# Optimization experiments

Measured on AMD Instinct MI355X. Metric: run time of the kernel, lower is better.

The kernel has to match this reference:

```python
import jax, jax.numpy as jnp
import numpy as np

B, S, E, H, V = 64, 256, 300, 300, 30000
R, NREL, RELD, POL = 512, 46, 50, 3


def setup_inputs() -> dict:
    rng = np.random.RandomState(0)
    text_indices = rng.randint(1, V, size=(B, S)).astype(np.int64)  # all nonzero -> text_len == S
    aspect_indices = rng.randint(1, V, size=(B, 4)).astype(np.int64)  # aspect_len == 4
    left_indices = np.zeros((B, 64), dtype=np.int64)
    for b in range(B):
        li = rng.randint(1, 61)
        left_indices[b, :li] = rng.randint(1, V, size=li)
    # distinct, row-major-sorted (head, behead) pairs so nonzero(adj) order matches relation order
    flat = np.stack([np.sort(rng.choice(S * S, size=R, replace=False)) for _ in range(B)])
    head = (flat // S).astype(np.int64)
    behead = (flat % S).astype(np.int64)
    relation = rng.randint(1, NREL, size=(B, R)).astype(np.int64)  # all nonzero
    adj = np.zeros((B, S, S), dtype=np.float32)
    adj[np.arange(B)[:, None], head, behead] = 1.0

    def p(*shape):
        return jnp.asarray((rng.randn(*shape) * 0.02).astype(np.float32))

    rel_embed = np.asarray(rng.randn(NREL, RELD) * 0.02, dtype=np.float32)
    rel_embed[0] = 0.0  # padding_idx=0
    return dict(
        text_indices=jnp.asarray(text_indices),
        aspect_indices=jnp.asarray(aspect_indices),
        left_indices=jnp.asarray(left_indices),
        adj=jnp.asarray(adj),
        head_vector=jnp.asarray(head),
        behead_vector=jnp.asarray(behead),
        relation_vector=jnp.asarray(relation),
        embed_table=p(V, E),
        rel_embed=jnp.asarray(rel_embed),
        Wf_ih=p(4 * H, E), Wf_hh=p(4 * H, H), bf=p(4 * H),
        Wb_ih=p(4 * H, E), Wb_hh=p(4 * H, H), bb=p(4 * H),
        bil_W=p(4 * H, RELD), bil_b=p(1),
        gc1_W=p(2 * H, 2 * H), gc1_b=p(2 * H),
        gc2_W=p(2 * H, 2 * H), gc2_b=p(2 * H),
        fc_W=p(2 * H, POL), fc_b=p(POL),
    )


def _lstm_dir(x_tbe, W_ih, W_hh, b):
    # x_tbe: [S, B, E]; PyTorch gate order i, f, g, o
    def step(carry, xt):
        h, c = carry
        g = xt @ W_ih.T + h @ W_hh.T + b
        i, f, gg, o = jnp.split(g, 4, axis=-1)
        c = jax.nn.sigmoid(f) * c + jax.nn.sigmoid(i) * jnp.tanh(gg)
        h = jax.nn.sigmoid(o) * jnp.tanh(c)
        return (h, c), h
    nb = x_tbe.shape[1]
    init = (jnp.zeros((nb, H), x_tbe.dtype), jnp.zeros((nb, H), x_tbe.dtype))
    _, hs = jax.lax.scan(step, init, x_tbe)
    return hs


def _bilstm(x, Wf_ih, Wf_hh, bf, Wb_ih, Wb_hh, bb):
    xt = jnp.swapaxes(x, 0, 1)  # [S, B, E]; all lengths == S by construction
    hf = _lstm_dir(xt, Wf_ih, Wf_hh, bf)
    hb = _lstm_dir(xt[::-1], Wb_ih, Wb_hh, bb)[::-1]
    return jnp.swapaxes(jnp.concatenate([hf, hb], axis=-1), 0, 1)  # [B, S, 2H]


def _pos_weight(x, l0, l1, text_len, aspect_len):
    j = jnp.arange(S, dtype=jnp.float32)[None, :]
    tl = text_len.astype(jnp.float32)[:, None]
    ctx = tl - aspect_len.astype(jnp.float32)[:, None]
    l0f = l0.astype(jnp.float32)[:, None]
    l1f = l1.astype(jnp.float32)[:, None]
    w = jnp.where(j < l0f, 1.0 - (l0f - j) / ctx,
        jnp.where(j <= l1f, 0.0,
        jnp.where(j < tl, 1.0 - (j - l1f) / ctx, 0.0)))
    return w[:, :, None] * x


def _gcn(text, adj, W, b):
    hidden = text @ W
    denom = jnp.sum(adj, axis=2, keepdims=True) + 1.0
    return jnp.matmul(adj, hidden) / denom + b


def reference(text_indices, aspect_indices, left_indices, adj, head_vector,
              behead_vector, relation_vector, embed_table, rel_embed,
              Wf_ih, Wf_hh, bf, Wb_ih, Wb_hh, bb, bil_W, bil_b,
              gc1_W, gc1_b, gc2_W, gc2_b, fc_W, fc_b):
    text_len = jnp.sum(text_indices != 0, axis=-1)
    aspect_len = jnp.sum(aspect_indices != 0, axis=-1)
    left_len = jnp.sum(left_indices != 0, axis=-1)
    l0 = left_len
    l1 = left_len + aspect_len - 1

    text = embed_table[text_indices]  # dropout is identity in eval mode
    text_out = _bilstm(text, Wf_ih, Wf_hh, bf, Wb_ih, Wb_hh, bb)  # [B, S, 2H]

    # --- word_relation_word: gather head/tail nodes, bilinear score, scatter into adj ---
    bidx = jnp.arange(B)[:, None]
    ind = (relation_vector != 0).astype(text_out.dtype)[:, :, None]
    node1 = jnp.where(ind != 0, text_out[bidx, head_vector], ind)   # [B, R, 2H]
    node2 = jnp.where(ind != 0, text_out[bidx, behead_vector], ind)
    ww = jnp.concatenate([node1, node2], axis=-1)                   # [B, R, 4H]
    ef = rel_embed[relation_vector]                                 # [B, R, 50]
    score = jax.nn.sigmoid(jnp.einsum('bri,ij,brj->br', ww, bil_W, ef) + bil_b[0])
    # nonzero(adj) positions == (head, behead) pairs in row-major order by construction
    adj = adj.at[bidx, head_vector, behead_vector].set(score)

    x = jax.nn.relu(_gcn(_pos_weight(text_out, l0, l1, text_len, aspect_len), adj, gc1_W, gc1_b))
    x = jax.nn.relu(_gcn(_pos_weight(x, l0, l1, text_len, aspect_len), adj, gc2_W, gc2_b))

    j = jnp.arange(S)[None, :]
    m = ((j >= l0[:, None]) & (j <= l1[:, None])).astype(x.dtype)[:, :, None]
    x = m * x
    alpha_mat = jnp.matmul(x, jnp.swapaxes(text_out, 1, 2))  # [B, S, S]
    alpha = jax.nn.softmax(jnp.sum(alpha_mat, axis=1, keepdims=True), axis=2)
    x = jnp.matmul(alpha, text_out).squeeze(1)               # [B, 2H]
    return x @ fc_W + fc_b
```

## Files before the change

kernel.cpp:

```cpp
#include <hip/hip_runtime.h>
#include <hip/hip_bf16.h>

typedef __hip_bfloat16 bf16;
using f32x4 = __attribute__((ext_vector_type(4))) float;
using s16x8 = __attribute__((ext_vector_type(8))) short;

#define DEV __device__ __forceinline__
DEV float bf2f(bf16 x) { return __bfloat162float(x); }
DEV bf16  f2bf(float x) { return __float2bfloat16(x); }
DEV ushort f2bu(float x) { bf16 h = __float2bfloat16(x); return *(ushort*)&h; }
DEV float fsig(float x)  { return 1.f / (1.f + __expf(-x)); }
DEV float ftanh(float x) {
    float xc = fminf(fmaxf(x, -15.f), 15.f);
    float e = __expf(2.f * xc);
    return (e - 1.f) / (e + 1.f);
}

#define BB 64
#define SS 256
#define EE 300
#define HH 300
#define H2 600
#define G4 1200
#define RR 512
#define VV 30000

#define NWG 25
#define CPW 12
#define HPITCH 304

#define SLOTSZ   19660800ul
#define GATES_SZ 39321600ul
#define OFF_TEXT  39321600ul
#define OFF_ADJ   78643200ul
#define OFF_P     87031808ul
#define OFF_DENOM 87252608ul
#define OFF_POSW  87318144ul
#define OFF_L0L1  87383680ul
#define OFF_W1T   87384704ul
#define OFF_W2T   88104704ul
#define OFF_HG    88824704ul
#define OFF_FLAGS 88980352ul
#define SEQ_END   89045888ul
#define CONC_END  128367488ul

struct __attribute__((packed, aligned(4))) u16x8v { ushort v[8]; };

__global__ void k_init_denom(float* denom) {
    int i = blockIdx.x * 256 + threadIdx.x;
    if (i < BB * SS) denom[i] = 1.f;
}

__global__ void k_lengths(const int* __restrict__ text_idx,
                          const int* __restrict__ aspect_idx,
                          const int* __restrict__ left_idx,
                          int* __restrict__ l0l1, float* __restrict__ posw) {
    int b = blockIdx.x, tid = threadIdx.x;
    __shared__ int cnt[3];
    if (tid < 3) cnt[tid] = 0;
    __syncthreads();
    if (text_idx[b * SS + tid] != 0) atomicAdd(&cnt[0], 1);
    if (tid < 4 && aspect_idx[b * 4 + tid] != 0) atomicAdd(&cnt[1], 1);
    if (tid < 64 && left_idx[b * 64 + tid] != 0) atomicAdd(&cnt[2], 1);
    __syncthreads();
    int tl = cnt[0], al = cnt[1], ll = cnt[2];
    int l0 = ll, l1 = ll + al - 1;
    if (tid == 0) { l0l1[b * 2] = l0; l0l1[b * 2 + 1] = l1; }
    float ctx = fmaxf((float)(tl - al), 1.f);
    float j = (float)tid, l0f = (float)l0, l1f = (float)l1, tlf = (float)tl;
    float w;
    if (j < l0f)       w = 1.f - (l0f - j) / ctx;
    else if (j <= l1f) w = 0.f;
    else if (j < tlf)  w = 1.f - (j - l1f) / ctx;
    else               w = 0.f;
    posw[b * SS + tid] = w;
}

__global__ void k_P(const float* __restrict__ bilW, const float* __restrict__ relE,
                    float* __restrict__ P) {
    int id = blockIdx.x * 256 + threadIdx.x;
    if (id >= G4 * 46) return;
    int i = id / 46, r = id % 46;
    float s = 0.f;
    for (int j = 0; j < 50; ++j) s += bilW[i * 50 + j] * relE[r * 50 + j];
    P[id] = s;
}

__global__ void k_transpose600(const float* __restrict__ W, bf16* __restrict__ WT) {
    int id = blockIdx.x * 256 + threadIdx.x;
    if (id >= H2 * H2) return;
    int n = id / H2, k = id % H2;
    WT[id] = f2bf(W[k * H2 + n]);
}

__global__ void k_pw1(const float* __restrict__ text_out, const float* __restrict__ posw,
                      bf16* __restrict__ pw1) {
    int id = blockIdx.x * 256 + threadIdx.x;
    if (id >= 16384 * H2) return;
    int m = id / H2;
    pw1[id] = f2bf(posw[m] * text_out[id]);
}

template<int EPI, bool GATHER_A, bool BATCHED, bool CVT>
__global__ __launch_bounds__(256) void gemm_bt(
    const void* __restrict__ Abv, const void* __restrict__ Bbv,
    int M, int N, int K, int lda, int ldb, long sA, long sB,
    const int* __restrict__ gidx,
    const float* __restrict__ bias0,
    const float* __restrict__ denom, const float* __restrict__ posw,
    bf16* __restrict__ Cbf, int ldc)
{
    __shared__ __align__(16) ushort As[128 * 40];
    __shared__ __align__(16) ushort Bs[128 * 40];
    const int tid  = threadIdx.x;
    const int lane = tid & 63, wave = tid >> 6;
    const int wm = (wave >> 1) * 64, wn = (wave & 1) * 64;
    const int mt = blockIdx.x * 128, nt = blockIdx.y * 128;
    const int z  = BATCHED ? blockIdx.z : 0;

    const int srow = tid >> 1;
    const int kseg = (tid & 1) * 16;
    long arow = mt + srow;
    if (GATHER_A) {
        int g = gidx[mt + srow];
        if (g < 0 || g >= VV) g = 0;
        arow = g;
    }
    const int nrow = nt + srow;
    const bool bval = nrow < N;
    const int nrc = bval ? nrow : 0;

    const ushort* Ap16 = nullptr; const ushort* Bp16 = nullptr;
    const float*  Ap32 = nullptr; const float*  Bp32 = nullptr;
    if (CVT) {
        Ap32 = (const float*)Abv + (BATCHED ? (long)z * sA : 0l) + arow * (long)lda;
        Bp32 = (const float*)Bbv + (BATCHED ? (long)z * sB : 0l) + (long)nrc * ldb;
    } else {
        Ap16 = (const ushort*)Abv + (BATCHED ? (long)z * sA : 0l) + arow * (long)lda;
        Bp16 = (const ushort*)Bbv + (BATCHED ? (long)z * sB : 0l) + (long)nrc * ldb;
    }

    f32x4 acc[4][4];
#pragma unroll
    for (int i = 0; i < 4; ++i)
#pragma unroll
        for (int j = 0; j < 4; ++j) acc[i][j] = (f32x4){0.f, 0.f, 0.f, 0.f};

    for (int k0 = 0; k0 < K; k0 += 32) {
        __syncthreads();
#pragma unroll
        for (int hv = 0; hv < 2; ++hv) {
            const int kk = k0 + kseg + hv * 8;
            union { ushort u[8]; uint4 q; } ta, tb;
            if (CVT) {
                if (kk + 8 <= K) {
                    float4 f0 = *(const float4*)(Ap32 + kk);
                    float4 f1 = *(const float4*)(Ap32 + kk + 4);
                    ta.u[0] = f2bu(f0.x); ta.u[1] = f2bu(f0.y); ta.u[2] = f2bu(f0.z); ta.u[3] = f2bu(f0.w);
                    ta.u[4] = f2bu(f1.x); ta.u[5] = f2bu(f1.y); ta.u[6] = f2bu(f1.z); ta.u[7] = f2bu(f1.w);
                } else {
#pragma unroll
                    for (int i2 = 0; i2 < 8; ++i2) ta.u[i2] = (kk + i2 < K) ? f2bu(Ap32[kk + i2]) : (ushort)0;
                }
                if (bval && kk + 8 <= K) {
                    float4 f0 = *(const float4*)(Bp32 + kk);
                    float4 f1 = *(const float4*)(Bp32 + kk + 4);
                    tb.u[0] = f2bu(f0.x); tb.u[1] = f2bu(f0.y); tb.u[2] = f2bu(f0.z); tb.u[3] = f2bu(f0.w);
                    tb.u[4] = f2bu(f1.x); tb.u[5] = f2bu(f1.y); tb.u[6] = f2bu(f1.z); tb.u[7] = f2bu(f1.w);
                } else {
#pragma unroll
                    for (int i2 = 0; i2 < 8; ++i2) tb.u[i2] = (bval && kk + i2 < K) ? f2bu(Bp32[kk + i2]) : (ushort)0;
                }
            } else {
                if (kk + 8 <= K) {
                    u16x8v v = *(const u16x8v*)(Ap16 + kk);
#pragma unroll
                    for (int i2 = 0; i2 < 8; ++i2) ta.u[i2] = v.v[i2];
                } else {
#pragma unroll
                    for (int i2 = 0; i2 < 8; ++i2) ta.u[i2] = (kk + i2 < K) ? Ap16[kk + i2] : (ushort)0;
                }
                if (bval && kk + 8 <= K) {
                    u16x8v v = *(const u16x8v*)(Bp16 + kk);
#pragma unroll
                    for (int i2 = 0; i2 < 8; ++i2) tb.u[i2] = v.v[i2];
                } else {
#pragma unroll
                    for (int i2 = 0; i2 < 8; ++i2) tb.u[i2] = (bval && kk + i2 < K) ? Bp16[kk + i2] : (ushort)0;
                }
            }
            *(uint4*)&As[srow * 40 + kseg + hv * 8] = ta.q;
            *(uint4*)&Bs[srow * 40 + kseg + hv * 8] = tb.q;
        }
        __syncthreads();
        s16x8 af[4], bfr[4];
#pragma unroll
        for (int i = 0; i < 4; ++i)
            af[i] = *(const s16x8*)&As[(wm + i * 16 + (lane & 15)) * 40 + (lane >> 4) * 8];
#pragma unroll
        for (int j = 0; j < 4; ++j)
            bfr[j] = *(const s16x8*)&Bs[(wn + j * 16 + (lane & 15)) * 40 + (lane >> 4) * 8];
#pragma unroll
        for (int i = 0; i < 4; ++i)
#pragma unroll
            for (int j = 0; j < 4; ++j)
                acc[i][j] = __builtin_amdgcn_mfma_f32_16x16x32_bf16(af[i], bfr[j], acc[i][j], 0, 0, 0);
    }

#pragma unroll
    for (int i = 0; i < 4; ++i) {
        const int rm = mt + wm + i * 16 + ((lane >> 4) * 4);
#pragma unroll
        for (int j = 0; j < 4; ++j) {
            const int gn = nt + wn + j * 16 + (lane & 15);
            if (gn >= N) continue;
#pragma unroll
            for (int r = 0; r < 4; ++r) {
                const int gm = rm + r;
                const float v = acc[i][j][r];
                if (EPI == 0) {
                    const int bb2 = gm >> 8, tt2 = gm & 255;
                    const int g3 = gn / 300, gr = gn % 300;
                    const int wgq = gr / 12, jq = gr % 12;
                    Cbf[(((long)tt2 * NWG + wgq) * BB + bb2) * 48 + g3 * 12 + jq]
                        = f2bf(v + bias0[gn]);
                } else if (EPI == 1) {
                    const int bb2 = gm >> 8, jj = gm & 255;
                    Cbf[((long)bb2 * H2 + gn) * SS + jj] = f2bf(v);
                } else {
                    const int grow = z * SS + gm;
                    float v2 = v / denom[grow] + bias0[gn];
                    v2 = fmaxf(v2, 0.f);
                    if (EPI == 2) v2 *= posw[grow];
                    Cbf[(long)grow * ldc + gn] = f2bf(v2);
                }
            }
        }
    }
}

__global__ __launch_bounds__(256, 1) void k_lstm_mfma(
    const bf16* __restrict__ gatesF, const bf16* __restrict__ gatesB,
    const float* __restrict__ WhhF, const float* __restrict__ WhhB,
    bf16* __restrict__ hgbase,
    int* __restrict__ flagbase,
    float* __restrict__ text_out, int dir_base)
{
    const int dir = dir_base + blockIdx.x / NWG;
    const int wg  = blockIdx.x % NWG;
    const ushort* gu  = (const ushort*)(dir ? gatesB : gatesF);
    const float*  Whh = dir ? WhhB : WhhF;
    ushort* hg   = (ushort*)hgbase + (long)dir * (2 * 64 * HPITCH);
    int*   flags = flagbase + dir * (256 * 32);

    const int tid = threadIdx.x, lane = tid & 63, wave = tid >> 6;
    __shared__ float cbuf[64 * CPW];

    const int nl15 = lane & 15;
    const int kq = lane >> 4;
    const int gI = nl15 & 3;
    s16x8 Bfrag[3][10];
#pragma unroll
    for (int tt = 0; tt < 3; ++tt) {
        const int j = (tt * 16 + nl15) >> 2;
        const float* wrow = Whh + ((long)(gI * HH + wg * CPW + j)) * HH;
        const int kb = kq * 8;
        for (int ss = 0; ss < 10; ++ss) {
            union { ushort u[8]; s16x8 v; } tb;
#pragma unroll
            for (int e = 0; e < 8; ++e) {
                const int k = ss * 32 + kb + e;
                tb.u[e] = (k < HH) ? f2bu(wrow[k]) : (ushort)0;
            }
            Bfrag[tt][ss] = tb.v;
        }
    }
    for (int i = tid; i < 64 * CPW; i += 256) cbuf[i] = 0.f;
    __syncthreads();

    const int am = wave * 16 + nl15;

    ushort gcur[3][4], gnxt[3][4];
    {
        const int tcur = dir ? (SS - 1) : 0;
#pragma unroll
        for (int tt = 0; tt < 3; ++tt) {
            const int col48 = gI * 12 + ((tt * 16 + nl15) >> 2);
#pragma unroll
            for (int r = 0; r < 4; ++r) {
                const int mb = wave * 16 + (kq << 2) + r;
                gcur[tt][r] = gu[(((long)tcur * NWG + wg) * BB + mb) * 48 + col48];
            }
        }
    }

    for (int s = 0; s < SS; ++s) {
        const int t = dir ? (SS - 1 - s) : s;
        const int rb = s & 1;
        unsigned long long hq[20];
        {
            const unsigned long long* src =
                (const unsigned long long*)(hg + rb * (64 * HPITCH)) + (long)am * 76;
#pragma unroll
            for (int ss = 0; ss < 10; ++ss) {
                hq[2 * ss]     = __hip_atomic_load(&src[ss * 8 + kq * 2],
                                                   __ATOMIC_RELAXED, __HIP_MEMORY_SCOPE_AGENT);
                hq[2 * ss + 1] = __hip_atomic_load(&src[ss * 8 + kq * 2 + 1],
                                                   __ATOMIC_RELAXED, __HIP_MEMORY_SCOPE_AGENT);
            }
        }
        f32x4 acc[3];
#pragma unroll
        for (int tt = 0; tt < 3; ++tt) acc[tt] = (f32x4){0.f, 0.f, 0.f, 0.f};
#pragma unroll
        for (int ss = 0; ss < 10; ++ss) {
            union { unsigned long long q[2]; s16x8 v; } ua;
            ua.q[0] = hq[2 * ss]; ua.q[1] = hq[2 * ss + 1];
#pragma unroll
            for (int tt = 0; tt < 3; ++tt)
                acc[tt] = __builtin_amdgcn_mfma_f32_16x16x32_bf16(ua.v, Bfrag[tt][ss], acc[tt], 0, 0, 0);
        }
        ushort* hw = hg + (rb ^ 1) * (64 * HPITCH);
#pragma unroll
        for (int tt = 0; tt < 3; ++tt) {
            const int j = (tt * 16 + nl15) >> 2;
            const int hc = wg * CPW + j;
#pragma unroll
            for (int r = 0; r < 4; ++r) {
                const int mb = wave * 16 + (kq << 2) + r;
                const bf16 gb = *(const bf16*)&gcur[tt][r];
                const float val = acc[tt][r] + bf2f(gb);
                const float a = (gI == 2) ? ftanh(val) : fsig(val);
                const float v1 = __shfl_xor(a, 1);
                const float v2 = __shfl_xor(a, 2);
                const float v3 = __shfl_xor(a, 3);
                if (gI == 0) {
                    const int ci = mb * CPW + j;
                    const float c = v1 * cbuf[ci] + a * v2;
                    cbuf[ci] = c;
                    const float h = v3 * ftanh(c);
                    bf16 hb = f2bf(h);
                    __hip_atomic_store(&hw[mb * HPITCH + hc], *(ushort*)&hb,
                                       __ATOMIC_RELAXED, __HIP_MEMORY_SCOPE_AGENT);
                    text_out[((long)(mb * SS + t)) * H2 + dir * HH + hc] = h;
                }
            }
        }
        if (s == SS - 1) break;
        __syncthreads();
        if (tid == 0)
            __hip_atomic_store(&flags[s * 32 + wg], 1, __ATOMIC_RELAXED, __HIP_MEMORY_SCOPE_AGENT);
        {
            const int tn = dir ? (SS - 2 - s) : (s + 1);
#pragma unroll
            for (int tt = 0; tt < 3; ++tt) {
                const int col48 = gI * 12 + ((tt * 16 + nl15) >> 2);
#pragma unroll
                for (int r = 0; r < 4; ++r) {
                    const int mb = wave * 16 + (kq << 2) + r;
                    gnxt[tt][r] = gu[(((long)tn * NWG + wg) * BB + mb) * 48 + col48];
                }
            }
        }
        if (tid < NWG) {
            while (__hip_atomic_load(&flags[s * 32 + tid], __ATOMIC_RELAXED,
                                     __HIP_MEMORY_SCOPE_AGENT) == 0) { }
        }
        __syncthreads();
#pragma unroll
        for (int tt = 0; tt < 3; ++tt)
#pragma unroll
            for (int r = 0; r < 4; ++r) gcur[tt][r] = gnxt[tt][r];
    }
}

__global__ void k_scores(const float* __restrict__ text_out, const float* __restrict__ P,
                         const int* __restrict__ head, const int* __restrict__ behead,
                         const int* __restrict__ rel, const float* __restrict__ bil_b,
                         bf16* __restrict__ adj, float* __restrict__ denom)
{
    const int gw = (blockIdx.x * blockDim.x + threadIdx.x) >> 6;
    const int lane = threadIdx.x & 63;
    if (gw >= BB * RR) return;
    const int b = gw >> 9, r = gw & 511;
    int rl = rel[b * RR + r];     if (rl < 0 || rl > 45) rl = 0;
    int hd = head[b * RR + r]   & 255;
    int bh = behead[b * RR + r] & 255;
    const float* n1 = text_out + ((long)(b * SS + hd)) * H2;
    const float* n2 = text_out + ((long)(b * SS + bh)) * H2;
    float part = 0.f;
    for (int i = lane; i < H2; i += 64) {
        part += n1[i] * P[(long)i * 46 + rl];
        part += n2[i] * P[(long)(H2 + i) * 46 + rl];
    }
    for (int off = 32; off; off >>= 1) part += __shfl_down(part, off);
    if (lane == 0) {
        const float sc = 1.f / (1.f + expf(-(part + bil_b[0])));
        adj[((long)(b * SS + hd)) * SS + bh] = f2bf(sc);
        atomicAdd(&denom[b * SS + hd], sc);
    }
}

__global__ __launch_bounds__(256) void k_attn(
    const float* __restrict__ text_out, const bf16* __restrict__ x2,
    const int* __restrict__ l0l1, const float* __restrict__ fcW,
    const float* __restrict__ fcb, float* __restrict__ out)
{
    const int b = blockIdx.x, tid = threadIdx.x;
    const int wave = tid >> 6, lane = tid & 63;
    __shared__ float xs[H2];
    __shared__ float sc[SS];
    __shared__ float red[16];
    const int l0 = l0l1[b * 2], l1 = l0l1[b * 2 + 1];
    for (int n = tid; n < H2; n += 256) {
        float s = 0.f;
        for (int i = l0; i <= l1 && i < SS; ++i) s += bf2f(x2[((long)(b * SS + i)) * H2 + n]);
        xs[n] = s;
    }
    __syncthreads();
    for (int j = wave; j < SS; j += 4) {
        const float* row = text_out + ((long)(b * SS + j)) * H2;
        float p = 0.f;
        for (int n = lane; n < H2; n += 64) p += xs[n] * row[n];
        for (int off = 32; off; off >>= 1) p += __shfl_down(p, off);
        if (lane == 0) sc[j] = p;
    }
    __syncthreads();
    const float v = sc[tid];
    float mx = v;
    for (int off = 32; off; off >>= 1) mx = fmaxf(mx, __shfl_down(mx, off));
    if (lane == 0) red[wave] = mx;
    __syncthreads();
    if (tid == 0) red[8] = fmaxf(fmaxf(red[0], red[1]), fmaxf(red[2], red[3]));
    __syncthreads();
    const float e = expf(v - red[8]);
    sc[tid] = e;
    float sm = e;
    for (int off = 32; off; off >>= 1) sm += __shfl_down(sm, off);
    if (lane == 0) red[wave] = sm;
    __syncthreads();
    if (tid == 0) red[9] = red[0] + red[1] + red[2] + red[3];
    __syncthreads();
    const float inv = 1.f / red[9];
    for (int n = tid; n < H2; n += 256) {
        float a = 0.f;
        for (int j = 0; j < SS; ++j) a += sc[j] * text_out[((long)(b * SS + j)) * H2 + n];
        xs[n] = a * inv;
    }
    __syncthreads();
    if (wave < 3) {
        float p = 0.f;
        for (int n = lane; n < H2; n += 64) p += xs[n] * fcW[n * 3 + wave];
        for (int off = 32; off; off >>= 1) p += __shfl_down(p, off);
        if (lane == 0) out[b * 3 + wave] = p + fcb[wave];
    }
}

extern "C" void kernel_launch(void* const* d_in, const int* in_sizes, int n_in,
                              void* d_out, int out_size, void* d_ws, size_t ws_size,
                              hipStream_t stream) {
    const int*   text_idx   = (const int*)d_in[0];
    const int*   aspect_idx = (const int*)d_in[1];
    const int*   left_idx   = (const int*)d_in[2];
    const int*   head       = (const int*)d_in[4];
    const int*   behead     = (const int*)d_in[5];
    const int*   rel        = (const int*)d_in[6];
    const float* embed      = (const float*)d_in[7];
    const float* relE       = (const float*)d_in[8];
    const float* Wf_ih      = (const float*)d_in[9];
    const float* Wf_hh      = (const float*)d_in[10];
    const float* bf_b       = (const float*)d_in[11];
    const float* Wb_ih      = (const float*)d_in[12];
    const float* Wb_hh      = (const float*)d_in[13];
    const float* bb_b       = (const float*)d_in[14];
    const float* bilW       = (const float*)d_in[15];
    const float* bilb       = (const float*)d_in[16];
    const float* gc1W       = (const float*)d_in[17];
    const float* gc1b       = (const float*)d_in[18];
    const float* gc2W       = (const float*)d_in[19];
    const float* gc2b       = (const float*)d_in[20];
    const float* fcW        = (const float*)d_in[21];
    const float* fcb        = (const float*)d_in[22];

    const bool  conc  = ws_size >= CONC_END;
    const size_t base2 = conc ? GATES_SZ : 0ul;

    char* ws = (char*)d_ws;
    bf16*  gatesF   = (bf16*)(ws);
    bf16*  gatesB   = conc ? (bf16*)(ws + GATES_SZ) : gatesF;
    bf16*  slot0bf  = (bf16*)(ws);
    bf16*  slot1bf  = (bf16*)(ws + SLOTSZ);
    float* text_out = (float*)(ws + OFF_TEXT  + base2);
    bf16*  adjw     = (bf16*)(ws + OFF_ADJ    + base2);
    float* P        = (float*)(ws + OFF_P     + base2);
    float* denom    = (float*)(ws + OFF_DENOM + base2);
    float* posw     = (float*)(ws + OFF_POSW  + base2);
    int*   l0l1     = (int*)(ws + OFF_L0L1    + base2);
    bf16*  W1T      = (bf16*)(ws + OFF_W1T    + base2);
    bf16*  W2T      = (bf16*)(ws + OFF_W2T    + base2);
    bf16*  hgbase   = (bf16*)(ws + OFF_HG     + base2);
    int*   flagbase = (int*)(ws + OFF_FLAGS   + base2);

    dim3 blk(256);

    hipMemsetAsync(adjw, 0, (size_t)BB * SS * SS * 2, stream);
    hipMemsetAsync(hgbase, 0, 155648 + 65536, stream);
    k_init_denom<<<64, blk, 0, stream>>>(denom);
    k_lengths<<<64, blk, 0, stream>>>(text_idx, aspect_idx, left_idx, l0l1, posw);
    k_P<<<(G4 * 46 + 255) / 256, blk, 0, stream>>>(bilW, relE, P);
    k_transpose600<<<(H2 * H2 + 255) / 256, blk, 0, stream>>>(gc1W, W1T);
    k_transpose600<<<(H2 * H2 + 255) / 256, blk, 0, stream>>>(gc2W, W2T);

    if (conc) {
        gemm_bt<0, true, false, true><<<dim3(128, 10), blk, 0, stream>>>(
            embed, Wf_ih, 16384, G4, EE, EE, EE, 0, 0,
            text_idx, bf_b, nullptr, nullptr, gatesF, G4);
        gemm_bt<0, true, false, true><<<dim3(128, 10), blk, 0, stream>>>(
            embed, Wb_ih, 16384, G4, EE, EE, EE, 0, 0,
            text_idx, bb_b, nullptr, nullptr, gatesB, G4);
        k_lstm_mfma<<<2 * NWG, blk, 0, stream>>>(
            gatesF, gatesB, Wf_hh, Wb_hh, hgbase, flagbase, text_out, 0);
    } else {
        gemm_bt<0, true, false, true><<<dim3(128, 10), blk, 0, stream>>>(
            embed, Wf_ih, 16384, G4, EE, EE, EE, 0, 0,
            text_idx, bf_b, nullptr, nullptr, gatesF, G4);
        k_lstm_mfma<<<NWG, blk, 0, stream>>>(
            gatesF, gatesB, Wf_hh, Wb_hh, hgbase, flagbase, text_out, 0);
        gemm_bt<0, true, false, true><<<dim3(128, 10), blk, 0, stream>>>(
            embed, Wb_ih, 16384, G4, EE, EE, EE, 0, 0,
            text_idx, bb_b, nullptr, nullptr, gatesB, G4);
        k_lstm_mfma<<<NWG, blk, 0, stream>>>(
            gatesF, gatesB, Wf_hh, Wb_hh, hgbase, flagbase, text_out, 1);
    }

    k_scores<<<(BB * RR * 64 + 255) / 256, blk, 0, stream>>>(
        text_out, P, head, behead, rel, bilb, adjw, denom);
    k_pw1<<<(16384 * H2 + 255) / 256, blk, 0, stream>>>(text_out, posw, slot0bf);

    gemm_bt<1, false, false, false><<<dim3(128, 5), blk, 0, stream>>>(
        slot0bf, W1T, 16384, H2, H2, H2, H2, 0, 0,
        nullptr, nullptr, nullptr, nullptr, slot1bf, 0);
    gemm_bt<2, false, true, false><<<dim3(2, 5, 64), blk, 0, stream>>>(
        adjw, slot1bf, SS, H2, SS, SS, SS, (long)SS * SS, (long)H2 * SS,
        nullptr, gc1b, denom, posw, slot0bf, H2);
    gemm_bt<1, false, false, false><<<dim3(128, 5), blk, 0, stream>>>(
        slot0bf, W2T, 16384, H2, H2, H2, H2, 0, 0,
        nullptr, nullptr, nullptr, nullptr, slot1bf, 0);
    gemm_bt<3, false, true, false><<<dim3(2, 5, 64), blk, 0, stream>>>(
        adjw, slot1bf, SS, H2, SS, SS, SS, (long)SS * SS, (long)H2 * SS,
        nullptr, gc2b, denom, posw, slot0bf, H2);

    k_attn<<<64, blk, 0, stream>>>(text_out, slot0bf, l0l1, fcW, fcb, (float*)d_out);
}
```

Before: 2.087 ms.

## Fuse setup kernels, merge gate GEMMs, fold pos-weight into GEMM, register LSTM cell

Folds the denom init into k_lengths and merges the two weight transposes into one launch. The forward and backward input-gate GEMMs become a single launch over 2*G4 columns, with per-column routing of bias and destination. The separate k_pw1 pass goes away: posw scaling and the bf16 conversion now happen in the first GCN GEMM's A-load through a new ASCALE path. In the LSTM, cell state moves from shared memory into registers, and the flag signal is raised before the text_out global stores so peers can proceed sooner. These changes cut launches and one full activation round trip, at the cost of more template complexity and more register pressure in the LSTM.

```diff
diff --git a/kernel.cpp b/kernel.cpp
--- a/kernel.cpp
+++ b/kernel.cpp
@@ -46,15 +46,11 @@
 
 struct __attribute__((packed, aligned(4))) u16x8v { ushort v[8]; };
 
-__global__ void k_init_denom(float* denom) {
-    int i = blockIdx.x * 256 + threadIdx.x;
-    if (i < BB * SS) denom[i] = 1.f;
-}
-
 __global__ void k_lengths(const int* __restrict__ text_idx,
                           const int* __restrict__ aspect_idx,
                           const int* __restrict__ left_idx,
-                          int* __restrict__ l0l1, float* __restrict__ posw) {
+                          int* __restrict__ l0l1, float* __restrict__ posw,
+                          float* __restrict__ denom) {
     int b = blockIdx.x, tid = threadIdx.x;
     __shared__ int cnt[3];
     if (tid < 3) cnt[tid] = 0;
@@ -74,6 +70,7 @@
     else if (j < tlf)  w = 1.f - (j - l1f) / ctx;
     else               w = 0.f;
     posw[b * SS + tid] = w;
+    denom[b * SS + tid] = 1.f;
 }
 
 __global__ void k_P(const float* __restrict__ bilW, const float* __restrict__ relE,
@@ -86,29 +83,26 @@
     P[id] = s;
 }
 
-__global__ void k_transpose600(const float* __restrict__ W, bf16* __restrict__ WT) {
+__global__ void k_transpose2(const float* __restrict__ Wa, const float* __restrict__ Wb,
+                             bf16* __restrict__ Ta, bf16* __restrict__ Tb) {
     int id = blockIdx.x * 256 + threadIdx.x;
-    if (id >= H2 * H2) return;
-    int n = id / H2, k = id % H2;
-    WT[id] = f2bf(W[k * H2 + n]);
-}
-
-__global__ void k_pw1(const float* __restrict__ text_out, const float* __restrict__ posw,
-                      bf16* __restrict__ pw1) {
-    int id = blockIdx.x * 256 + threadIdx.x;
-    if (id >= 16384 * H2) return;
-    int m = id / H2;
-    pw1[id] = f2bf(posw[m] * text_out[id]);
-}
-
-template<int EPI, bool GATHER_A, bool BATCHED, bool CVT>
+    if (id >= 2 * H2 * H2) return;
+    const float* W = (id < H2 * H2) ? Wa : Wb;
+    bf16* T = (id < H2 * H2) ? Ta : Tb;
+    int l = (id < H2 * H2) ? id : id - H2 * H2;
+    int n = l / H2, k = l % H2;
+    T[l] = f2bf(W[k * H2 + n]);
+}
+
+template<int EPI, bool GATHER_A, bool BATCHED, bool CVTA, bool CVTB, bool ASCALE>
 __global__ __launch_bounds__(256) void gemm_bt(
-    const void* __restrict__ Abv, const void* __restrict__ Bbv,
+    const void* __restrict__ Abv, const void* __restrict__ Bbv, const void* __restrict__ B2v,
     int M, int N, int K, int lda, int ldb, long sA, long sB,
     const int* __restrict__ gidx,
-    const float* __restrict__ bias0,
+    const float* __restrict__ bias0, const float* __restrict__ bias1,
+    const float* __restrict__ ascale,
     const float* __restrict__ denom, const float* __restrict__ posw,
-    bf16* __restrict__ Cbf, int ldc)
+    bf16* __restrict__ Cbf, bf16* __restrict__ Cbf2, int ldc)
 {
     __shared__ __align__(16) ushort As[128 * 40];
     __shared__ __align__(16) ushort Bs[128 * 40];
@@ -132,13 +126,22 @@
 
     const ushort* Ap16 = nullptr; const ushort* Bp16 = nullptr;
     const float*  Ap32 = nullptr; const float*  Bp32 = nullptr;
-    if (CVT) {
+    if (CVTA) {
         Ap32 = (const float*)Abv + (BATCHED ? (long)z * sA : 0l) + arow * (long)lda;
-        Bp32 = (const float*)Bbv + (BATCHED ? (long)z * sB : 0l) + (long)nrc * ldb;
     } else {
         Ap16 = (const ushort*)Abv + (BATCHED ? (long)z * sA : 0l) + arow * (long)lda;
+    }
+    if (CVTB) {
+        if (EPI == 0) {
+            Bp32 = (nrc < G4) ? (const float*)Bbv + (long)nrc * ldb
+                              : (const float*)B2v + (long)(nrc - G4) * ldb;
+        } else {
+            Bp32 = (const float*)Bbv + (BATCHED ? (long)z * sB : 0l) + (long)nrc * ldb;
+        }
+    } else {
         Bp16 = (const ushort*)Bbv + (BATCHED ? (long)z * sB : 0l) + (long)nrc * ldb;
     }
+    const float asc = ASCALE ? ascale[arow] : 1.f;
 
     f32x4 acc[4][4];
 #pragma unroll
@@ -152,16 +155,30 @@
         for (int hv = 0; hv < 2; ++hv) {
             const int kk = k0 + kseg + hv * 8;
             union { ushort u[8]; uint4 q; } ta, tb;
-            if (CVT) {
+            if (CVTA) {
                 if (kk + 8 <= K) {
                     float4 f0 = *(const float4*)(Ap32 + kk);
                     float4 f1 = *(const float4*)(Ap32 + kk + 4);
-                    ta.u[0] = f2bu(f0.x); ta.u[1] = f2bu(f0.y); ta.u[2] = f2bu(f0.z); ta.u[3] = f2bu(f0.w);
-                    ta.u[4] = f2bu(f1.x); ta.u[5] = f2bu(f1.y); ta.u[6] = f2bu(f1.z); ta.u[7] = f2bu(f1.w);
+                    ta.u[0] = f2bu(asc * f0.x); ta.u[1] = f2bu(asc * f0.y);
+                    ta.u[2] = f2bu(asc * f0.z); ta.u[3] = f2bu(asc * f0.w);
+                    ta.u[4] = f2bu(asc * f1.x); ta.u[5] = f2bu(asc * f1.y);
+                    ta.u[6] = f2bu(asc * f1.z); ta.u[7] = f2bu(asc * f1.w);
                 } else {
 #pragma unroll
-                    for (int i2 = 0; i2 < 8; ++i2) ta.u[i2] = (kk + i2 < K) ? f2bu(Ap32[kk + i2]) : (ushort)0;
-                }
+                    for (int i2 = 0; i2 < 8; ++i2)
+                        ta.u[i2] = (kk + i2 < K) ? f2bu(asc * Ap32[kk + i2]) : (ushort)0;
+                }
+            } else {
+                if (kk + 8 <= K) {
+                    u16x8v v = *(const u16x8v*)(Ap16 + kk);
+#pragma unroll
+                    for (int i2 = 0; i2 < 8; ++i2) ta.u[i2] = v.v[i2];
+                } else {
+#pragma unroll
+                    for (int i2 = 0; i2 < 8; ++i2) ta.u[i2] = (kk + i2 < K) ? Ap16[kk + i2] : (ushort)0;
+                }
+            }
+            if (CVTB) {
                 if (bval && kk + 8 <= K) {
                     float4 f0 = *(const float4*)(Bp32 + kk);
                     float4 f1 = *(const float4*)(Bp32 + kk + 4);
@@ -169,17 +186,10 @@
                     tb.u[4] = f2bu(f1.x); tb.u[5] = f2bu(f1.y); tb.u[6] = f2bu(f1.z); tb.u[7] = f2bu(f1.w);
                 } else {
 #pragma unroll
-                    for (int i2 = 0; i2 < 8; ++i2) tb.u[i2] = (bval && kk + i2 < K) ? f2bu(Bp32[kk + i2]) : (ushort)0;
+                    for (int i2 = 0; i2 < 8; ++i2)
+                        tb.u[i2] = (bval && kk + i2 < K) ? f2bu(Bp32[kk + i2]) : (ushort)0;
                 }
             } else {
-                if (kk + 8 <= K) {
-                    u16x8v v = *(const u16x8v*)(Ap16 + kk);
-#pragma unroll
-                    for (int i2 = 0; i2 < 8; ++i2) ta.u[i2] = v.v[i2];
-                } else {
-#pragma unroll
-                    for (int i2 = 0; i2 < 8; ++i2) ta.u[i2] = (kk + i2 < K) ? Ap16[kk + i2] : (ushort)0;
-                }
                 if (bval && kk + 8 <= K) {
                     u16x8v v = *(const u16x8v*)(Bp16 + kk);
 #pragma unroll
@@ -220,10 +230,13 @@
                 const float v = acc[i][j][r];
                 if (EPI == 0) {
                     const int bb2 = gm >> 8, tt2 = gm & 255;
-                    const int g3 = gn / 300, gr = gn % 300;
+                    bf16* dst = Cbf; int gl = gn; float bia;
+                    if (gn < G4) { bia = bias0[gn]; }
+                    else { dst = Cbf2; gl = gn - G4; bia = bias1[gl]; }
+                    const int g3 = gl / 300, gr = gl % 300;
                     const int wgq = gr / 12, jq = gr % 12;
-                    Cbf[(((long)tt2 * NWG + wgq) * BB + bb2) * 48 + g3 * 12 + jq]
-                        = f2bf(v + bias0[gn]);
+                    dst[(((long)tt2 * NWG + wgq) * BB + bb2) * 48 + g3 * 12 + jq]
+                        = f2bf(v + bia);
                 } else if (EPI == 1) {
                     const int bb2 = gm >> 8, jj = gm & 255;
                     Cbf[((long)bb2 * H2 + gn) * SS + jj] = f2bf(v);
@@ -254,11 +267,10 @@
     int*   flags = flagbase + dir * (256 * 32);
 
     const int tid = threadIdx.x, lane = tid & 63, wave = tid >> 6;
-    __shared__ float cbuf[64 * CPW];
-
     const int nl15 = lane & 15;
     const int kq = lane >> 4;
     const int gI = nl15 & 3;
+
     s16x8 Bfrag[3][10];
 #pragma unroll
     for (int tt = 0; tt < 3; ++tt) {
@@ -275,8 +287,11 @@
             Bfrag[tt][ss] = tb.v;
         }
     }
-    for (int i = tid; i < 64 * CPW; i += 256) cbuf[i] = 0.f;
-    __syncthreads();
+    float cval[3][4];
+#pragma unroll
+    for (int tt = 0; tt < 3; ++tt)
+#pragma unroll
+        for (int r = 0; r < 4; ++r) cval[tt][r] = 0.f;
 
     const int am = wave * 16 + nl15;
 
@@ -321,6 +336,7 @@
                 acc[tt] = __builtin_amdgcn_mfma_f32_16x16x32_bf16(ua.v, Bfrag[tt][ss], acc[tt], 0, 0, 0);
         }
         ushort* hw = hg + (rb ^ 1) * (64 * HPITCH);
+        float hval[3][4];
 #pragma unroll
         for (int tt = 0; tt < 3; ++tt) {
             const int j = (tt * 16 + nl15) >> 2;
@@ -335,21 +351,32 @@
                 const float v2 = __shfl_xor(a, 2);
                 const float v3 = __shfl_xor(a, 3);
                 if (gI == 0) {
-                    const int ci = mb * CPW + j;
-                    const float c = v1 * cbuf[ci] + a * v2;
-                    cbuf[ci] = c;
+                    const float c = v1 * cval[tt][r] + a * v2;
+                    cval[tt][r] = c;
                     const float h = v3 * ftanh(c);
+                    hval[tt][r] = h;
                     bf16 hb = f2bf(h);
                     __hip_atomic_store(&hw[mb * HPITCH + hc], *(ushort*)&hb,
                                        __ATOMIC_RELAXED, __HIP_MEMORY_SCOPE_AGENT);
-                    text_out[((long)(mb * SS + t)) * H2 + dir * HH + hc] = h;
-                }
+                }
+            }
+        }
+        if (s < SS - 1) {
+            __syncthreads();
+            if (tid == 0)
+                __hip_atomic_store(&flags[s * 32 + wg], 1, __ATOMIC_RELAXED, __HIP_MEMORY_SCOPE_AGENT);
+        }
+#pragma unroll
+        for (int tt = 0; tt < 3; ++tt) {
+            const int hc = wg * CPW + ((tt * 16 + nl15) >> 2);
+#pragma unroll
+            for (int r = 0; r < 4; ++r) {
+                const int mb = wave * 16 + (kq << 2) + r;
+                if (gI == 0)
+                    text_out[((long)(mb * SS + t)) * H2 + dir * HH + hc] = hval[tt][r];
             }
         }
         if (s == SS - 1) break;
-        __syncthreads();
-        if (tid == 0)
-            __hip_atomic_store(&flags[s * 32 + wg], 1, __ATOMIC_RELAXED, __HIP_MEMORY_SCOPE_AGENT);
         {
             const int tn = dir ? (SS - 2 - s) : (s + 1);
 #pragma unroll
@@ -505,50 +532,44 @@
 
     hipMemsetAsync(adjw, 0, (size_t)BB * SS * SS * 2, stream);
     hipMemsetAsync(hgbase, 0, 155648 + 65536, stream);
-    k_init_denom<<<64, blk, 0, stream>>>(denom);
-    k_lengths<<<64, blk, 0, stream>>>(text_idx, aspect_idx, left_idx, l0l1, posw);
+    k_lengths<<<64, blk, 0, stream>>>(text_idx, aspect_idx, left_idx, l0l1, posw, denom);
     k_P<<<(G4 * 46 + 255) / 256, blk, 0, stream>>>(bilW, relE, P);
-    k_transpose600<<<(H2 * H2 + 255) / 256, blk, 0, stream>>>(gc1W, W1T);
-    k_transpose600<<<(H2 * H2 + 255) / 256, blk, 0, stream>>>(gc2W, W2T);
+    k_transpose2<<<(2 * H2 * H2 + 255) / 256, blk, 0, stream>>>(gc1W, gc2W, W1T, W2T);
 
     if (conc) {
-        gemm_bt<0, true, false, true><<<dim3(128, 10), blk, 0, stream>>>(
-            embed, Wf_ih, 16384, G4, EE, EE, EE, 0, 0,
-            text_idx, bf_b, nullptr, nullptr, gatesF, G4);
-        gemm_bt<0, true, false, true><<<dim3(128, 10), blk, 0, stream>>>(
-            embed, Wb_ih, 16384, G4, EE, EE, EE, 0, 0,
-            text_idx, bb_b, nullptr, nullptr, gatesB, G4);
+        gemm_bt<0, true, false, true, true, false><<<dim3(128, 19), blk, 0, stream>>>(
+            embed, Wf_ih, Wb_ih, 16384, 2 * G4, EE, EE, EE, 0, 0,
+            text_idx, bf_b, bb_b, nullptr, nullptr, nullptr, gatesF, gatesB, 0);
         k_lstm_mfma<<<2 * NWG, blk, 0, stream>>>(
             gatesF, gatesB, Wf_hh, Wb_hh, hgbase, flagbase, text_out, 0);
     } else {
-        gemm_bt<0, true, false, true><<<dim3(128, 10), blk, 0, stream>>>(
-            embed, Wf_ih, 16384, G4, EE, EE, EE, 0, 0,
-            text_idx, bf_b, nullptr, nullptr, gatesF, G4);
+        gemm_bt<0, true, false, true, true, false><<<dim3(128, 10), blk, 0, stream>>>(
+            embed, Wf_ih, Wf_ih, 16384, G4, EE, EE, EE, 0, 0,
+            text_idx, bf_b, bf_b, nullptr, nullptr, nullptr, gatesF, gatesF, 0);
         k_lstm_mfma<<<NWG, blk, 0, stream>>>(
             gatesF, gatesB, Wf_hh, Wb_hh, hgbase, flagbase, text_out, 0);
-        gemm_bt<0, true, false, true><<<dim3(128, 10), blk, 0, stream>>>(
-            embed, Wb_ih, 16384, G4, EE, EE, EE, 0, 0,
-            text_idx, bb_b, nullptr, nullptr, gatesB, G4);
+        gemm_bt<0, true, false, true, true, false><<<dim3(128, 10), blk, 0, stream>>>(
+            embed, Wb_ih, Wb_ih, 16384, G4, EE, EE, EE, 0, 0,
+            text_idx, bb_b, bb_b, nullptr, nullptr, nullptr, gatesB, gatesB, 0);
         k_lstm_mfma<<<NWG, blk, 0, stream>>>(
             gatesF, gatesB, Wf_hh, Wb_hh, hgbase, flagbase, text_out, 1);
     }
 
     k_scores<<<(BB * RR * 64 + 255) / 256, blk, 0, stream>>>(
         text_out, P, head, behead, rel, bilb, adjw, denom);
-    k_pw1<<<(16384 * H2 + 255) / 256, blk, 0, stream>>>(text_out, posw, slot0bf);
-
-    gemm_bt<1, false, false, false><<<dim3(128, 5), blk, 0, stream>>>(
-        slot0bf, W1T, 16384, H2, H2, H2, H2, 0, 0,
-        nullptr, nullptr, nullptr, nullptr, slot1bf, 0);
-    gemm_bt<2, false, true, false><<<dim3(2, 5, 64), blk, 0, stream>>>(
-        adjw, slot1bf, SS, H2, SS, SS, SS, (long)SS * SS, (long)H2 * SS,
-        nullptr, gc1b, denom, posw, slot0bf, H2);
-    gemm_bt<1, false, false, false><<<dim3(128, 5), blk, 0, stream>>>(
-        slot0bf, W2T, 16384, H2, H2, H2, H2, 0, 0,
-        nullptr, nullptr, nullptr, nullptr, slot1bf, 0);
-    gemm_bt<3, false, true, false><<<dim3(2, 5, 64), blk, 0, stream>>>(
-        adjw, slot1bf, SS, H2, SS, SS, SS, (long)SS * SS, (long)H2 * SS,
-        nullptr, gc2b, denom, posw, slot0bf, H2);
+
+    gemm_bt<1, false, false, true, false, true><<<dim3(128, 5), blk, 0, stream>>>(
+        text_out, W1T, nullptr, 16384, H2, H2, H2, H2, 0, 0,
+        nullptr, nullptr, nullptr, posw, nullptr, nullptr, slot1bf, nullptr, 0);
+    gemm_bt<2, false, true, false, false, false><<<dim3(2, 5, 64), blk, 0, stream>>>(
+        adjw, slot1bf, nullptr, SS, H2, SS, SS, SS, (long)SS * SS, (long)H2 * SS,
+        nullptr, gc1b, nullptr, nullptr, denom, posw, slot0bf, nullptr, H2);
+    gemm_bt<1, false, false, false, false, false><<<dim3(128, 5), blk, 0, stream>>>(
+        slot0bf, W2T, nullptr, 16384, H2, H2, H2, H2, 0, 0,
+        nullptr, nullptr, nullptr, nullptr, nullptr, nullptr, slot1bf, nullptr, 0);
+    gemm_bt<3, false, true, false, false, false><<<dim3(2, 5, 64), blk, 0, stream>>>(
+        adjw, slot1bf, nullptr, SS, H2, SS, SS, SS, (long)SS * SS, (long)H2 * SS,
+        nullptr, gc2b, nullptr, nullptr, denom, posw, slot0bf, nullptr, H2);
 
     k_attn<<<64, blk, 0, stream>>>(text_out, slot0bf, l0l1, fcW, fcb, (float*)d_out);
 }
```

Result: faster. 2.032 ms (-2.6%).
